# Kernel tuning notes

Measured on AMD Instinct MI355X. Metric: run time of the kernel, lower is better.

Reference implementation:

```python
import jax, jax.numpy as jnp
import numpy as np

NU, NI, D, E = 200_000, 100_000, 128, 600_000
EPS = 1e-5


def _linear(x, W, b):
    # torch nn.Linear: y = x @ W.T + b, W is [out, in]
    return x @ W.T + b


def _layer_norm(x, g, b):
    mu = jnp.mean(x, axis=-1, keepdims=True)
    var = jnp.mean((x - mu) ** 2, axis=-1, keepdims=True)
    return (x - mu) * jax.lax.rsqrt(var + EPS) * g + b


def _sym_norm_w(row, col, n_src, n_dst):
    ones = jnp.ones(row.shape, jnp.float32)
    deg_s = jax.ops.segment_sum(ones, row, num_segments=n_src)
    deg_d = jax.ops.segment_sum(ones, col, num_segments=n_dst)
    inv_s = jnp.where(deg_s > 0, deg_s ** -0.5, 0.0)
    inv_d = jnp.where(deg_d > 0, deg_d ** -0.5, 0.0)
    return inv_s[row] * inv_d[col]  # [E]


def _relation(x_src, row, col, n_dst, Wl, bl, Wf, bf):
    w = _sym_norm_w(row, col, x_src.shape[0], n_dst)
    m = x_src[row] * w[:, None]                      # gather + scale, [E, D]
    s = jax.ops.segment_sum(m, col, num_segments=n_dst)      # sum messages
    sq = jax.ops.segment_sum(m * m, col, num_segments=n_dst)  # sum of squares
    fm = 0.5 * (s * s - sq)                          # FM interaction
    return _linear(s, Wl, bl) + _linear(fm, Wf, bf)


def setup_inputs() -> dict:
    key = jax.random.key(0)
    ks = jax.random.split(key, 24)
    scale = 1.0 / np.sqrt(D)
    p = lambda k: jax.random.normal(k, (D, D), jnp.float32) * scale
    return {
        "h_user": jax.random.normal(ks[0], (NU, D), jnp.float32),
        "h_item": jax.random.normal(ks[1], (NI, D), jnp.float32),
        "ei_u2i_src": jax.random.randint(ks[2], (E,), 0, NU),
        "ei_u2i_dst": jax.random.randint(ks[3], (E,), 0, NI),
        "ei_i2u_src": jax.random.randint(ks[4], (E,), 0, NI),
        "ei_i2u_dst": jax.random.randint(ks[5], (E,), 0, NU),
        "Ws_user": p(ks[6]), "bs_user": jnp.zeros((D,), jnp.float32),
        "Ws_item": p(ks[7]), "bs_item": jnp.zeros((D,), jnp.float32),
        "Wlin_u2i": p(ks[8]), "blin_u2i": jnp.zeros((D,), jnp.float32),
        "Wfm_u2i": p(ks[9]), "bfm_u2i": jnp.zeros((D,), jnp.float32),
        "Wlin_i2u": p(ks[10]), "blin_i2u": jnp.zeros((D,), jnp.float32),
        "Wfm_i2u": p(ks[11]), "bfm_i2u": jnp.zeros((D,), jnp.float32),
        "g_user": jnp.ones((D,), jnp.float32), "be_user": jnp.zeros((D,), jnp.float32),
        "g_item": jnp.ones((D,), jnp.float32), "be_item": jnp.zeros((D,), jnp.float32),
    }


def reference(h_user, h_item, ei_u2i_src, ei_u2i_dst, ei_i2u_src, ei_i2u_dst,
              Ws_user, bs_user, Ws_item, bs_item,
              Wlin_u2i, blin_u2i, Wfm_u2i, bfm_u2i,
              Wlin_i2u, blin_i2u, Wfm_i2u, bfm_i2u,
              g_user, be_user, g_item, be_item):
    out_u = _linear(h_user, Ws_user, bs_user)
    out_i = _linear(h_item, Ws_item, bs_item)
    # edge type (user, rates, item): src=user, dst=item
    out_i = out_i + _relation(h_user, ei_u2i_src, ei_u2i_dst, NI,
                              Wlin_u2i, blin_u2i, Wfm_u2i, bfm_u2i)
    # edge type (item, rated_by, user): src=item, dst=user
    out_u = out_u + _relation(h_item, ei_i2u_src, ei_i2u_dst, NU,
                              Wlin_i2u, blin_i2u, Wfm_i2u, bfm_i2u)
    out_u = jax.nn.relu(_layer_norm(out_u, g_user, be_user))
    out_i = jax.nn.relu(_layer_norm(out_i, g_item, be_item))
    return out_u, out_i
```

## Files before the change

kernel.cpp:

```cpp
#include <hip/hip_runtime.h>
#include <hip/hip_bf16.h>

#define NU 200000
#define NI 100000
#define DD 128
#define EE 600000
#define CAP 32
#define N8U (NU * DD / 8)
#define N8I (NI * DD / 8)
#define N8W (DD * DD / 8)
#define NCONV (N8U + N8I + 6 * N8W)
#define NCB ((NCONV + 255) / 256)
#define NPB2 ((2 * EE + 255) / 256)
#define ZN4 ((2 * NU + 2 * NI) / 4)
#define NGAB ((NI + 3) / 4)
#define NGBB ((NU + 3) / 4)
#define NMA ((NI + 127) / 128)
#define NMB ((NU + 127) / 128)

typedef __attribute__((ext_vector_type(8))) short bf16x8;
typedef __attribute__((ext_vector_type(4))) float f32x4;

__device__ __forceinline__ unsigned short f2bf(float f) {
    unsigned int u = __float_as_uint(f);
    u += 0x7fff + ((u >> 16) & 1);
    return (unsigned short)(u >> 16);
}
__device__ __forceinline__ float bf2f(unsigned short h) {
    return __uint_as_float(((unsigned int)h) << 16);
}

__global__ void zero_kernel(int* __restrict__ z) {
    int i = blockIdx.x * blockDim.x + threadIdx.x;
    if (i < ZN4) ((int4*)z)[i] = make_int4(0, 0, 0, 0);
}

__global__ void convplace_kernel(
        const float* __restrict__ hu, const float* __restrict__ hi,
        const float* __restrict__ w0, const float* __restrict__ w1,
        const float* __restrict__ w2, const float* __restrict__ w3,
        const float* __restrict__ w4, const float* __restrict__ w5,
        unsigned short* __restrict__ hub, unsigned short* __restrict__ hib,
        unsigned short* __restrict__ wb,
        const int* __restrict__ srcA, const int* __restrict__ dstA,
        const int* __restrict__ srcB, const int* __restrict__ dstB,
        int* __restrict__ degAs, int* __restrict__ cntA, int* __restrict__ bktA,
        int* __restrict__ degBs, int* __restrict__ cntB, int* __restrict__ bktB) {
    int b = blockIdx.x;
    if (b < NPB2) {
        int e = b * 256 + threadIdx.x;
        if (e < EE) {
            int r = srcA[e], c = dstA[e];
            atomicAdd(&degAs[r], 1);
            int slot = atomicAdd(&cntA[c], 1);
            if (slot < CAP) bktA[c * CAP + slot] = r;
        } else if (e < 2 * EE) {
            int f = e - EE;
            int r = srcB[f], c = dstB[f];
            atomicAdd(&degBs[r], 1);
            int slot = atomicAdd(&cntB[c], 1);
            if (slot < CAP) bktB[c * CAP + slot] = r;
        }
        return;
    }
    int i = (b - NPB2) * 256 + threadIdx.x;
    if (i >= NCONV) return;
    const float* src; unsigned short* dst; int k;
    if (i < N8U) { src = hu; dst = hub; k = i; }
    else if (i < N8U + N8I) { src = hi; dst = hib; k = i - N8U; }
    else {
        int j = i - N8U - N8I;
        int wsel = j >> 11;
        k = j & (N8W - 1);
        src = (wsel == 0) ? w0 : (wsel == 1) ? w1 : (wsel == 2) ? w2
            : (wsel == 3) ? w3 : (wsel == 4) ? w4 : w5;
        dst = wb + wsel * DD * DD;
    }
    const float4* p = (const float4*)src + (size_t)k * 2;
    float4 v0 = p[0], v1 = p[1];
    union { unsigned short us[8]; uint4 u4; } r;
    r.us[0] = f2bf(v0.x); r.us[1] = f2bf(v0.y); r.us[2] = f2bf(v0.z); r.us[3] = f2bf(v0.w);
    r.us[4] = f2bf(v1.x); r.us[5] = f2bf(v1.y); r.us[6] = f2bf(v1.z); r.us[7] = f2bf(v1.w);
    ((uint4*)dst)[k] = r.u4;
}

__device__ __forceinline__ void gather_rows(const unsigned short* __restrict__ x,
                                            const int* __restrict__ cnt,
                                            const int* __restrict__ degS,
                                            const int* __restrict__ bkt,
                                            unsigned short* __restrict__ sOut,
                                            unsigned short* __restrict__ fmOut,
                                            int N, int bid) {
    int d = bid * 4 + (threadIdx.x >> 6);
    int lane = threadIdx.x & 63;
    if (d >= N) return;
    int cfull = cnt[d];
    int dg = min(cfull, CAP);
    float invD = (cfull > 0) ? rsqrtf((float)cfull) : 0.f;
    const int* brow = bkt + (size_t)d * CAP;
    float s0 = 0.f, s1 = 0.f, q0 = 0.f, q1 = 0.f;
    for (int j = 0; j < dg; j += 8) {
        int rem = dg - j;
        int4 iv0 = *(const int4*)(brow + j);
        int4 iv1 = *(const int4*)(brow + j + 4);
        int i0 = iv0.x;
        int i1 = (rem > 1) ? iv0.y : i0;
        int i2 = (rem > 2) ? iv0.z : i0;
        int i3 = (rem > 3) ? iv0.w : i0;
        int i4 = (rem > 4) ? iv1.x : i0;
        int i5 = (rem > 5) ? iv1.y : i0;
        int i6 = (rem > 6) ? iv1.z : i0;
        int i7 = (rem > 7) ? iv1.w : i0;
        float w0 = rsqrtf((float)degS[i0]) * invD;
        float w1 = (rem > 1) ? rsqrtf((float)degS[i1]) * invD : 0.f;
        float w2 = (rem > 2) ? rsqrtf((float)degS[i2]) * invD : 0.f;
        float w3 = (rem > 3) ? rsqrtf((float)degS[i3]) * invD : 0.f;
        float w4 = (rem > 4) ? rsqrtf((float)degS[i4]) * invD : 0.f;
        float w5 = (rem > 5) ? rsqrtf((float)degS[i5]) * invD : 0.f;
        float w6 = (rem > 6) ? rsqrtf((float)degS[i6]) * invD : 0.f;
        float w7 = (rem > 7) ? rsqrtf((float)degS[i7]) * invD : 0.f;
        unsigned int u0 = *(const unsigned int*)(x + (size_t)i0 * DD + lane * 2);
        unsigned int u1 = *(const unsigned int*)(x + (size_t)i1 * DD + lane * 2);
        unsigned int u2 = *(const unsigned int*)(x + (size_t)i2 * DD + lane * 2);
        unsigned int u3 = *(const unsigned int*)(x + (size_t)i3 * DD + lane * 2);
        unsigned int u4 = *(const unsigned int*)(x + (size_t)i4 * DD + lane * 2);
        unsigned int u5 = *(const unsigned int*)(x + (size_t)i5 * DD + lane * 2);
        unsigned int u6 = *(const unsigned int*)(x + (size_t)i6 * DD + lane * 2);
        unsigned int u7 = *(const unsigned int*)(x + (size_t)i7 * DD + lane * 2);
        float a, b;
        a = bf2f((unsigned short)(u0 & 0xffff)) * w0; b = bf2f((unsigned short)(u0 >> 16)) * w0;
        s0 += a; q0 += a * a; s1 += b; q1 += b * b;
        a = bf2f((unsigned short)(u1 & 0xffff)) * w1; b = bf2f((unsigned short)(u1 >> 16)) * w1;
        s0 += a; q0 += a * a; s1 += b; q1 += b * b;
        a = bf2f((unsigned short)(u2 & 0xffff)) * w2; b = bf2f((unsigned short)(u2 >> 16)) * w2;
        s0 += a; q0 += a * a; s1 += b; q1 += b * b;
        a = bf2f((unsigned short)(u3 & 0xffff)) * w3; b = bf2f((unsigned short)(u3 >> 16)) * w3;
        s0 += a; q0 += a * a; s1 += b; q1 += b * b;
        a = bf2f((unsigned short)(u4 & 0xffff)) * w4; b = bf2f((unsigned short)(u4 >> 16)) * w4;
        s0 += a; q0 += a * a; s1 += b; q1 += b * b;
        a = bf2f((unsigned short)(u5 & 0xffff)) * w5; b = bf2f((unsigned short)(u5 >> 16)) * w5;
        s0 += a; q0 += a * a; s1 += b; q1 += b * b;
        a = bf2f((unsigned short)(u6 & 0xffff)) * w6; b = bf2f((unsigned short)(u6 >> 16)) * w6;
        s0 += a; q0 += a * a; s1 += b; q1 += b * b;
        a = bf2f((unsigned short)(u7 & 0xffff)) * w7; b = bf2f((unsigned short)(u7 >> 16)) * w7;
        s0 += a; q0 += a * a; s1 += b; q1 += b * b;
    }
    float f0 = 0.5f * (s0 * s0 - q0), f1 = 0.5f * (s1 * s1 - q1);
    unsigned int spack = (unsigned int)f2bf(s0) | ((unsigned int)f2bf(s1) << 16);
    unsigned int fpack = (unsigned int)f2bf(f0) | ((unsigned int)f2bf(f1) << 16);
    *(unsigned int*)(sOut  + (size_t)d * DD + lane * 2) = spack;
    *(unsigned int*)(fmOut + (size_t)d * DD + lane * 2) = fpack;
}

__global__ __launch_bounds__(256) void gather2_kernel(
        const unsigned short* __restrict__ hub, const unsigned short* __restrict__ hib,
        const int* __restrict__ cntA, const int* __restrict__ degAs, const int* __restrict__ bktA,
        const int* __restrict__ cntB, const int* __restrict__ degBs, const int* __restrict__ bktB,
        unsigned short* __restrict__ sbA, unsigned short* __restrict__ fbA,
        unsigned short* __restrict__ sbB, unsigned short* __restrict__ fbB) {
    int b = blockIdx.x;
    if (b < NGAB) {
        gather_rows(hub, cntA, degAs, bktA, sbA, fbA, NI, b);
    } else {
        gather_rows(hib, cntB, degBs, bktB, sbB, fbB, NU, b - NGAB);
    }
}

__device__ __forceinline__ void gemm_ln_block(unsigned char* Wlds, int bid,
        const unsigned short* __restrict__ Xh,
        const unsigned short* __restrict__ Xs, const unsigned short* __restrict__ Xf,
        const unsigned short* __restrict__ W0, const unsigned short* __restrict__ W1,
        const unsigned short* __restrict__ W2,
        const float* __restrict__ B0, const float* __restrict__ B1,
        const float* __restrict__ B2,
        const float* __restrict__ g, const float* __restrict__ be,
        float* __restrict__ out, int N) {
    int tid  = threadIdx.x;
    int wv   = tid >> 6, lane = tid & 63;
    int rlo  = lane & 15, kg = lane >> 4;
    int rowbase = bid * 128 + wv * 32;
    int ar0 = min(rowbase + rlo,      N - 1);
    int ar1 = min(rowbase + 16 + rlo, N - 1);

    f32x4 acc[2][8];
    #pragma unroll
    for (int rt = 0; rt < 2; ++rt)
        #pragma unroll
        for (int jt = 0; jt < 8; ++jt) acc[rt][jt] = (f32x4){0.f, 0.f, 0.f, 0.f};

    const unsigned short* Xp[3] = {Xh, Xs, Xf};
    const unsigned short* Wp[3] = {W0, W1, W2};
    size_t a0off = (size_t)ar0 * DD + kg * 8;
    size_t a1off = (size_t)ar1 * DD + kg * 8;
    #pragma unroll
    for (int s3 = 0; s3 < 3; ++s3) {
        const uint4* Wg = (const uint4*)Wp[s3];
        #pragma unroll
        for (int it = 0; it < 8; ++it) {
            int slot = it * 256 + tid;
            int row = slot >> 4, c = slot & 15;
            uint4 v = Wg[slot];
            int sc = c ^ (row & 7);
            *(uint4*)(Wlds + ((row << 8) + (sc << 4))) = v;
        }
        __syncthreads();
        const unsigned short* X = Xp[s3];
        #pragma unroll
        for (int ks = 0; ks < 4; ++ks) {
            bf16x8 bfr[8];
            #pragma unroll
            for (int jt = 0; jt < 8; ++jt) {
                int jrow = jt * 16 + rlo;
                int boff = (jrow << 8) + ((((ks << 2) + kg) ^ (jrow & 7)) << 4);
                bfr[jt] = *(const bf16x8*)(Wlds + boff);
            }
            bf16x8 a0 = *(const bf16x8*)(X + a0off + ks * 32);
            bf16x8 a1 = *(const bf16x8*)(X + a1off + ks * 32);
            #pragma unroll
            for (int jt = 0; jt < 8; ++jt)
                acc[0][jt] = __builtin_amdgcn_mfma_f32_16x16x32_bf16(a0, bfr[jt], acc[0][jt], 0, 0, 0);
            #pragma unroll
            for (int jt = 0; jt < 8; ++jt)
                acc[1][jt] = __builtin_amdgcn_mfma_f32_16x16x32_bf16(a1, bfr[jt], acc[1][jt], 0, 0, 0);
        }
        __syncthreads();
    }

    float bsum[8], gg[8], bb[8];
    #pragma unroll
    for (int jt = 0; jt < 8; ++jt) {
        int col = jt * 16 + rlo;
        bsum[jt] = B0[col] + B1[col] + B2[col];
        gg[jt] = g[col]; bb[jt] = be[col];
    }
    #pragma unroll
    for (int rt = 0; rt < 2; ++rt) {
        float s1[4] = {0.f, 0.f, 0.f, 0.f}, s2[4] = {0.f, 0.f, 0.f, 0.f};
        #pragma unroll
        for (int jt = 0; jt < 8; ++jt)
            #pragma unroll
            for (int r = 0; r < 4; ++r) {
                float v = acc[rt][jt][r] + bsum[jt];
                acc[rt][jt][r] = v;
                s1[r] += v;
                s2[r] += v * v;
            }
        #pragma unroll
        for (int m = 1; m < 16; m <<= 1)
            #pragma unroll
            for (int r = 0; r < 4; ++r) {
                s1[r] += __shfl_xor(s1[r], m);
                s2[r] += __shfl_xor(s2[r], m);
            }
        #pragma unroll
        for (int r = 0; r < 4; ++r) {
            int grow = rowbase + rt * 16 + kg * 4 + r;
            if (grow >= N) continue;
            float mu  = s1[r] * (1.f / 128.f);
            float var = s2[r] * (1.f / 128.f) - mu * mu;
            float inv = rsqrtf(var + 1e-5f);
            #pragma unroll
            for (int jt = 0; jt < 8; ++jt) {
                int col = jt * 16 + rlo;
                float o = (acc[rt][jt][r] - mu) * inv * gg[jt] + bb[jt];
                out[(size_t)grow * DD + col] = fmaxf(o, 0.f);
            }
        }
    }
}

__global__ __launch_bounds__(256) void gemm2_kernel(
        const unsigned short* __restrict__ hub, const unsigned short* __restrict__ hib,
        const unsigned short* __restrict__ sbA, const unsigned short* __restrict__ fbA,
        const unsigned short* __restrict__ sbB, const unsigned short* __restrict__ fbB,
        const unsigned short* __restrict__ WsU, const unsigned short* __restrict__ WsI,
        const unsigned short* __restrict__ WlA, const unsigned short* __restrict__ WfA,
        const unsigned short* __restrict__ WlB, const unsigned short* __restrict__ WfB,
        const float* __restrict__ bs_user, const float* __restrict__ bs_item,
        const float* __restrict__ blA, const float* __restrict__ bfA,
        const float* __restrict__ blB, const float* __restrict__ bfB,
        const float* __restrict__ g_user, const float* __restrict__ be_user,
        const float* __restrict__ g_item, const float* __restrict__ be_item,
        float* __restrict__ out_u, float* __restrict__ out_i) {
    __shared__ __align__(16) unsigned char Wlds[32768];
    int b = blockIdx.x;
    if (b < NMA) {
        gemm_ln_block(Wlds, b, hib, sbA, fbA, WsI, WlA, WfA,
                      bs_item, blA, bfA, g_item, be_item, out_i, NI);
    } else {
        gemm_ln_block(Wlds, b - NMA, hub, sbB, fbB, WsU, WlB, WfB,
                      bs_user, blB, bfB, g_user, be_user, out_u, NU);
    }
}

extern "C" void kernel_launch(void* const* d_in, const int* in_sizes, int n_in,
                              void* d_out, int out_size, void* d_ws, size_t ws_size,
                              hipStream_t stream) {
    const float* h_user   = (const float*)d_in[0];
    const float* h_item   = (const float*)d_in[1];
    const int*   u2i_src  = (const int*)d_in[2];
    const int*   u2i_dst  = (const int*)d_in[3];
    const int*   i2u_src  = (const int*)d_in[4];
    const int*   i2u_dst  = (const int*)d_in[5];
    const float* Ws_user  = (const float*)d_in[6];
    const float* bs_user  = (const float*)d_in[7];
    const float* Ws_item  = (const float*)d_in[8];
    const float* bs_item  = (const float*)d_in[9];
    const float* Wlin_u2i = (const float*)d_in[10];
    const float* blin_u2i = (const float*)d_in[11];
    const float* Wfm_u2i  = (const float*)d_in[12];
    const float* bfm_u2i  = (const float*)d_in[13];
    const float* Wlin_i2u = (const float*)d_in[14];
    const float* blin_i2u = (const float*)d_in[15];
    const float* Wfm_i2u  = (const float*)d_in[16];
    const float* bfm_i2u  = (const float*)d_in[17];
    const float* g_user   = (const float*)d_in[18];
    const float* be_user  = (const float*)d_in[19];
    const float* g_item   = (const float*)d_in[20];
    const float* be_item  = (const float*)d_in[21];

    float* out   = (float*)d_out;
    float* out_u = out;
    float* out_i = out + (size_t)NU * DD;

    char* wsb = (char*)d_ws;
    int* degAs = (int*)wsb;       wsb += sizeof(int) * NU;
    int* degBs = (int*)wsb;       wsb += sizeof(int) * NI;
    int* cntA  = (int*)wsb;       wsb += sizeof(int) * NI;
    int* cntB  = (int*)wsb;       wsb += sizeof(int) * NU;
    int* bktA  = (int*)wsb;       wsb += sizeof(int) * (size_t)NI * CAP;
    int* bktB  = (int*)wsb;       wsb += sizeof(int) * (size_t)NU * CAP;
    unsigned short* hub = (unsigned short*)wsb;  wsb += sizeof(short) * (size_t)NU * DD;
    unsigned short* hib = (unsigned short*)wsb;  wsb += sizeof(short) * (size_t)NI * DD;
    unsigned short* sbA = (unsigned short*)wsb;  wsb += sizeof(short) * (size_t)NI * DD;
    unsigned short* fbA = (unsigned short*)wsb;  wsb += sizeof(short) * (size_t)NI * DD;
    unsigned short* sbB = (unsigned short*)wsb;  wsb += sizeof(short) * (size_t)NU * DD;
    unsigned short* fbB = (unsigned short*)wsb;  wsb += sizeof(short) * (size_t)NU * DD;
    unsigned short* wb  = (unsigned short*)wsb;  wsb += sizeof(short) * 6 * DD * DD;
    unsigned short* WsU = wb;
    unsigned short* WsI = wb + 1 * DD * DD;
    unsigned short* WlA = wb + 2 * DD * DD;
    unsigned short* WfA = wb + 3 * DD * DD;
    unsigned short* WlB = wb + 4 * DD * DD;
    unsigned short* WfB = wb + 5 * DD * DD;

    zero_kernel<<<(ZN4 + 255) / 256, 256, 0, stream>>>(degAs);

    convplace_kernel<<<NPB2 + NCB, 256, 0, stream>>>(
        h_user, h_item, Ws_user, Ws_item, Wlin_u2i, Wfm_u2i, Wlin_i2u, Wfm_i2u,
        hub, hib, wb,
        u2i_src, u2i_dst, i2u_src, i2u_dst,
        degAs, cntA, bktA, degBs, cntB, bktB);

    gather2_kernel<<<NGAB + NGBB, 256, 0, stream>>>(
        hub, hib, cntA, degAs, bktA, cntB, degBs, bktB, sbA, fbA, sbB, fbB);

    gemm2_kernel<<<NMA + NMB, 256, 0, stream>>>(
        hub, hib, sbA, fbA, sbB, fbB,
        WsU, WsI, WlA, WfA, WlB, WfB,
        bs_user, bs_item, blin_u2i, bfm_u2i, blin_i2u, bfm_i2u,
        g_user, be_user, g_item, be_item, out_u, out_i);
}
```

Baseline: 453.3 us.

## Privatize edge bucketing per XCD with workgroup-scope atomics and a merge pass

Edge placement now writes to per-XCD private degree counters, counts and buckets (indexed by the hardware XCC id) using workgroup-scope atomics. A merge pass then sums the counters and concatenates the buckets, fused with the bf16 conversion kernel. The goal is to avoid costly device-scope atomics that contend across XCDs. In exchange it adds an extra kernel launch, a much larger zeroing pass (eight private copies) and extra bucket traffic. Workgroup-scope atomics on memory shared by several CUs of one XCD rely on L2 coherence, and the per-XCD cap of 16 may drop edges that the old cap of 32 kept.

```diff
diff --git a/kernel.cpp b/kernel.cpp
--- a/kernel.cpp
+++ b/kernel.cpp
@@ -6,13 +6,17 @@
 #define DD 128
 #define EE 600000
 #define CAP 32
+#define CAPX 16
+#define NXCD 8
 #define N8U (NU * DD / 8)
 #define N8I (NI * DD / 8)
 #define N8W (DD * DD / 8)
 #define NCONV (N8U + N8I + 6 * N8W)
 #define NCB ((NCONV + 255) / 256)
+#define NUB ((NU + 255) / 256)
+#define NIB ((NI + 255) / 256)
 #define NPB2 ((2 * EE + 255) / 256)
-#define ZN4 ((2 * NU + 2 * NI) / 4)
+#define ZPRIV4 ((NXCD * 2 * (NU + NI)) / 4)
 #define NGAB ((NI + 3) / 4)
 #define NGBB ((NU + 3) / 4)
 #define NMA ((NI + 127) / 128)
@@ -29,41 +33,97 @@
 __device__ __forceinline__ float bf2f(unsigned short h) {
     return __uint_as_float(((unsigned int)h) << 16);
 }
+__device__ __forceinline__ int xcc_id() {
+    unsigned x;
+    asm volatile("s_getreg_b32 %0, hwreg(HW_REG_XCC_ID)" : "=s"(x));
+    return (int)(x & 7);
+}
+__device__ __forceinline__ int atomic_inc_l2(int* p) {
+    return __hip_atomic_fetch_add(p, 1, __ATOMIC_RELAXED, __HIP_MEMORY_SCOPE_WORKGROUP);
+}
 
 __global__ void zero_kernel(int* __restrict__ z) {
     int i = blockIdx.x * blockDim.x + threadIdx.x;
-    if (i < ZN4) ((int4*)z)[i] = make_int4(0, 0, 0, 0);
-}
-
-__global__ void convplace_kernel(
+    if (i < ZPRIV4) ((int4*)z)[i] = make_int4(0, 0, 0, 0);
+}
+
+__global__ __launch_bounds__(256) void place2_priv_kernel(
+        const int* __restrict__ srcA, const int* __restrict__ dstA,
+        const int* __restrict__ srcB, const int* __restrict__ dstB,
+        int* __restrict__ degAs_p, int* __restrict__ cntA_p, int* __restrict__ bktA_p,
+        int* __restrict__ degBs_p, int* __restrict__ cntB_p, int* __restrict__ bktB_p) {
+    int e = blockIdx.x * 256 + threadIdx.x;
+    if (e >= 2 * EE) return;
+    int xcc = xcc_id();
+    if (e < EE) {
+        int r = srcA[e], c = dstA[e];
+        atomic_inc_l2(&degAs_p[xcc * NU + r]);
+        int slot = atomic_inc_l2(&cntA_p[xcc * NI + c]);
+        if (slot < CAPX) bktA_p[((size_t)(xcc * NI) + c) * CAPX + slot] = r;
+    } else {
+        int f = e - EE;
+        int r = srcB[f], c = dstB[f];
+        atomic_inc_l2(&degBs_p[xcc * NI + r]);
+        int slot = atomic_inc_l2(&cntB_p[xcc * NU + c]);
+        if (slot < CAPX) bktB_p[((size_t)(xcc * NU) + c) * CAPX + slot] = r;
+    }
+}
+
+__global__ void convmerge_kernel(
         const float* __restrict__ hu, const float* __restrict__ hi,
         const float* __restrict__ w0, const float* __restrict__ w1,
         const float* __restrict__ w2, const float* __restrict__ w3,
         const float* __restrict__ w4, const float* __restrict__ w5,
         unsigned short* __restrict__ hub, unsigned short* __restrict__ hib,
         unsigned short* __restrict__ wb,
-        const int* __restrict__ srcA, const int* __restrict__ dstA,
-        const int* __restrict__ srcB, const int* __restrict__ dstB,
-        int* __restrict__ degAs, int* __restrict__ cntA, int* __restrict__ bktA,
-        int* __restrict__ degBs, int* __restrict__ cntB, int* __restrict__ bktB) {
+        const int* __restrict__ degAs_p, const int* __restrict__ cntA_p,
+        const int* __restrict__ bktA_p,
+        const int* __restrict__ degBs_p, const int* __restrict__ cntB_p,
+        const int* __restrict__ bktB_p,
+        int* __restrict__ degAs, int* __restrict__ cntA, int* __restrict__ mcntA,
+        int* __restrict__ bktA,
+        int* __restrict__ degBs, int* __restrict__ cntB, int* __restrict__ mcntB,
+        int* __restrict__ bktB) {
     int b = blockIdx.x;
-    if (b < NPB2) {
-        int e = b * 256 + threadIdx.x;
-        if (e < EE) {
-            int r = srcA[e], c = dstA[e];
-            atomicAdd(&degAs[r], 1);
-            int slot = atomicAdd(&cntA[c], 1);
-            if (slot < CAP) bktA[c * CAP + slot] = r;
-        } else if (e < 2 * EE) {
-            int f = e - EE;
-            int r = srcB[f], c = dstB[f];
-            atomicAdd(&degBs[r], 1);
-            int slot = atomicAdd(&cntB[c], 1);
-            if (slot < CAP) bktB[c * CAP + slot] = r;
+    if (b < NUB) {
+        int u = b * 256 + threadIdx.x;
+        if (u >= NU) return;
+        int dsum = 0, tot = 0, off = 0;
+        #pragma unroll
+        for (int x = 0; x < NXCD; ++x) dsum += degAs_p[x * NU + u];
+        degAs[u] = dsum;
+        #pragma unroll
+        for (int x = 0; x < NXCD; ++x) {
+            int c = cntB_p[x * NU + u];
+            tot += c;
+            c = min(c, CAPX);
+            const int* bp = bktB_p + ((size_t)(x * NU) + u) * CAPX;
+            for (int k = 0; k < c && off < CAP; ++k) bktB[(size_t)u * CAP + off++] = bp[k];
         }
+        cntB[u] = tot;
+        mcntB[u] = off;
         return;
     }
-    int i = (b - NPB2) * 256 + threadIdx.x;
+    if (b < NUB + NIB) {
+        int i = (b - NUB) * 256 + threadIdx.x;
+        if (i >= NI) return;
+        int dsum = 0, tot = 0, off = 0;
+        #pragma unroll
+        for (int x = 0; x < NXCD; ++x) dsum += degBs_p[x * NI + i];
+        degBs[i] = dsum;
+        #pragma unroll
+        for (int x = 0; x < NXCD; ++x) {
+            int c = cntA_p[x * NI + i];
+            tot += c;
+            c = min(c, CAPX);
+            const int* bp = bktA_p + ((size_t)(x * NI) + i) * CAPX;
+            for (int k = 0; k < c && off < CAP; ++k) bktA[(size_t)i * CAP + off++] = bp[k];
+        }
+        cntA[i] = tot;
+        mcntA[i] = off;
+        return;
+    }
+    int i = (b - NUB - NIB) * 256 + threadIdx.x;
     if (i >= NCONV) return;
     const float* src; unsigned short* dst; int k;
     if (i < N8U) { src = hu; dst = hub; k = i; }
@@ -85,6 +145,7 @@
 }
 
 __device__ __forceinline__ void gather_rows(const unsigned short* __restrict__ x,
+                                            const int* __restrict__ mcnt,
                                             const int* __restrict__ cnt,
                                             const int* __restrict__ degS,
                                             const int* __restrict__ bkt,
@@ -94,8 +155,8 @@
     int d = bid * 4 + (threadIdx.x >> 6);
     int lane = threadIdx.x & 63;
     if (d >= N) return;
+    int dg = min(mcnt[d], CAP);
     int cfull = cnt[d];
-    int dg = min(cfull, CAP);
     float invD = (cfull > 0) ? rsqrtf((float)cfull) : 0.f;
     const int* brow = bkt + (size_t)d * CAP;
     float s0 = 0.f, s1 = 0.f, q0 = 0.f, q1 = 0.f;
@@ -154,15 +215,17 @@
 
 __global__ __launch_bounds__(256) void gather2_kernel(
         const unsigned short* __restrict__ hub, const unsigned short* __restrict__ hib,
-        const int* __restrict__ cntA, const int* __restrict__ degAs, const int* __restrict__ bktA,
-        const int* __restrict__ cntB, const int* __restrict__ degBs, const int* __restrict__ bktB,
+        const int* __restrict__ mcntA, const int* __restrict__ cntA,
+        const int* __restrict__ degAs, const int* __restrict__ bktA,
+        const int* __restrict__ mcntB, const int* __restrict__ cntB,
+        const int* __restrict__ degBs, const int* __restrict__ bktB,
         unsigned short* __restrict__ sbA, unsigned short* __restrict__ fbA,
         unsigned short* __restrict__ sbB, unsigned short* __restrict__ fbB) {
     int b = blockIdx.x;
     if (b < NGAB) {
-        gather_rows(hub, cntA, degAs, bktA, sbA, fbA, NI, b);
+        gather_rows(hub, mcntA, cntA, degAs, bktA, sbA, fbA, NI, b);
     } else {
-        gather_rows(hib, cntB, degBs, bktB, sbB, fbB, NU, b - NGAB);
+        gather_rows(hib, mcntB, cntB, degBs, bktB, sbB, fbB, NU, b - NGAB);
     }
 }
 
@@ -324,12 +387,20 @@
     float* out_i = out + (size_t)NU * DD;
 
     char* wsb = (char*)d_ws;
+    int* degAs_p = (int*)wsb;     wsb += sizeof(int) * NXCD * NU;
+    int* degBs_p = (int*)wsb;     wsb += sizeof(int) * NXCD * NI;
+    int* cntA_p  = (int*)wsb;     wsb += sizeof(int) * NXCD * NI;
+    int* cntB_p  = (int*)wsb;     wsb += sizeof(int) * NXCD * NU;
     int* degAs = (int*)wsb;       wsb += sizeof(int) * NU;
     int* degBs = (int*)wsb;       wsb += sizeof(int) * NI;
     int* cntA  = (int*)wsb;       wsb += sizeof(int) * NI;
     int* cntB  = (int*)wsb;       wsb += sizeof(int) * NU;
-    int* bktA  = (int*)wsb;       wsb += sizeof(int) * (size_t)NI * CAP;
-    int* bktB  = (int*)wsb;       wsb += sizeof(int) * (size_t)NU * CAP;
+    int* mcntA = (int*)wsb;       wsb += sizeof(int) * NI;
+    int* mcntB = (int*)wsb;       wsb += sizeof(int) * NU;
+    int* bktA_p = (int*)wsb;      wsb += sizeof(int) * (size_t)NXCD * NI * CAPX;
+    int* bktB_p = (int*)wsb;      wsb += sizeof(int) * (size_t)NXCD * NU * CAPX;
+    int* bktA   = (int*)wsb;      wsb += sizeof(int) * (size_t)NI * CAP;
+    int* bktB   = (int*)wsb;      wsb += sizeof(int) * (size_t)NU * CAP;
     unsigned short* hub = (unsigned short*)wsb;  wsb += sizeof(short) * (size_t)NU * DD;
     unsigned short* hib = (unsigned short*)wsb;  wsb += sizeof(short) * (size_t)NI * DD;
     unsigned short* sbA = (unsigned short*)wsb;  wsb += sizeof(short) * (size_t)NI * DD;
@@ -344,16 +415,21 @@
     unsigned short* WlB = wb + 4 * DD * DD;
     unsigned short* WfB = wb + 5 * DD * DD;
 
-    zero_kernel<<<(ZN4 + 255) / 256, 256, 0, stream>>>(degAs);
-
-    convplace_kernel<<<NPB2 + NCB, 256, 0, stream>>>(
+    zero_kernel<<<(ZPRIV4 + 255) / 256, 256, 0, stream>>>(degAs_p);
+
+    place2_priv_kernel<<<NPB2, 256, 0, stream>>>(
+        u2i_src, u2i_dst, i2u_src, i2u_dst,
+        degAs_p, cntA_p, bktA_p, degBs_p, cntB_p, bktB_p);
+
+    convmerge_kernel<<<NUB + NIB + NCB, 256, 0, stream>>>(
         h_user, h_item, Ws_user, Ws_item, Wlin_u2i, Wfm_u2i, Wlin_i2u, Wfm_i2u,
         hub, hib, wb,
-        u2i_src, u2i_dst, i2u_src, i2u_dst,
-        degAs, cntA, bktA, degBs, cntB, bktB);
+        degAs_p, cntA_p, bktA_p, degBs_p, cntB_p, bktB_p,
+        degAs, cntA, mcntA, bktA, degBs, cntB, mcntB, bktB);
 
     gather2_kernel<<<NGAB + NGBB, 256, 0, stream>>>(
-        hub, hib, cntA, degAs, bktA, cntB, degBs, bktB, sbA, fbA, sbB, fbB);
+        hub, hib, mcntA, cntA, degAs, bktA, mcntB, cntB, degBs, bktB,
+        sbA, fbA, sbB, fbB);
 
     gemm2_kernel<<<NMA + NMB, 256, 0, stream>>>(
         hub, hib, sbA, fbA, sbB, fbB,
```

After: 487.8 us. +7.6%, slower.
